# Optimization experiments

Hardware: AMD Instinct MI355X
Metric: run time of the kernel (lower is better)

The kernel has to match this reference:

```python
import jax, jax.numpy as jnp
import numpy as np

E = 23   # unique_experts_num
K = 3    # act_experts_num
D = 1024 # in_features
H = 768  # hidden_features (0.75 * dim, per MOEBlock mlp_ratio)


def setup_inputs() -> dict:
    key = jax.random.key(0)
    ks = jax.random.split(key, 12)
    s_in = 1.0 / np.sqrt(D)
    s_hid = 1.0 / np.sqrt(H)
    x = jax.random.normal(ks[0], (4, 1024, D), dtype=jnp.float32)
    gate_W = jax.random.normal(ks[1], (D, E), dtype=jnp.float32) * s_in
    gate_b = jnp.zeros((E,), jnp.float32)
    bias = jnp.zeros((E,), jnp.float32)  # registered buffer, init to zeros
    W1 = jax.random.normal(ks[2], (E, D, H), dtype=jnp.float32) * s_in
    b1 = jnp.zeros((E, H), jnp.float32)
    W2 = jax.random.normal(ks[3], (E, H, D), dtype=jnp.float32) * s_hid
    b2 = jnp.zeros((E, D), jnp.float32)
    sW1 = jax.random.normal(ks[4], (D, H), dtype=jnp.float32) * s_in
    sb1 = jnp.zeros((H,), jnp.float32)
    sW2 = jax.random.normal(ks[5], (H, D), dtype=jnp.float32) * s_hid
    sb2 = jnp.zeros((D,), jnp.float32)
    return {"x": x, "gate_W": gate_W, "gate_b": gate_b, "bias": bias,
            "W1": W1, "b1": b1, "W2": W2, "b2": b2,
            "sW1": sW1, "sb1": sb1, "sW2": sW2, "sb2": sb2}


def reference(x, gate_W, gate_b, bias, W1, b1, W2, b2, sW1, sb1, sW2, sb2):
    o_shape = x.shape
    xt = x.reshape(-1, o_shape[-1])          # [T, D]
    T = xt.shape[0]

    # gating: sigmoid gate, top-k indices chosen on (gate + bias), weights gathered from gate
    gate = jax.nn.sigmoid(xt @ gate_W + gate_b)            # [T, E]
    _, top_idx = jax.lax.top_k(gate + bias, K)             # [T, K]
    top_w = jnp.take_along_axis(gate, top_idx, axis=-1)    # [T, K]
    top_w = top_w / jnp.sum(top_w, axis=-1, keepdims=True)

    # combine matrix: C[t, e] = normalized gate weight if e in top-k of token t else 0
    C = jnp.zeros((T, E), xt.dtype).at[jnp.arange(T)[:, None], top_idx].set(top_w)

    # all-expert dense compute (math-equivalent to dispatch/compute/combine)
    h = jax.nn.gelu(jnp.einsum('td,edh->eth', xt, W1) + b1[:, None, :], approximate=False)
    y = jnp.einsum('eth,ehd->etd', h, W2) + b2[:, None, :]  # [E, T, D]
    moe_out = jnp.einsum('etd,te->td', y, C)                # weighted combine

    # shared expert applied to every token
    shared = jax.nn.gelu(xt @ sW1 + sb1, approximate=False) @ sW2 + sb2
    out = shared + moe_out

    # aux load-balance loss
    gate_norm = gate / jnp.sum(gate, axis=-1, keepdims=True)
    P = jnp.mean(gate_norm, axis=0)                          # [E]
    counts = jnp.sum(jax.nn.one_hot(top_idx, E, dtype=jnp.float32), axis=(0, 1))  # [E]
    F = E * counts / (K * T)
    aux_loss = jnp.sum(P * F)

    return out.reshape(o_shape), aux_loss, counts.astype(jnp.int32)
```

## Files before the change

### kernel.cpp

```cpp
#include <hip/hip_runtime.h>
#include <math.h>

#define TT 4096
#define DD 1024
#define HH 768
#define NE 23
#define NG 24
#define BM 128
#define BN 128
#define BK 64
#define MAXT 160
#define KB1 16
#define KB2 12
#define NY1 6
#define NY2 8
#define NWG1 (MAXT*NY1)
#define NWG2 (MAXT*NY2)

#define WS_CURS   0
#define WS_COUNTS 512
#define WS_PSUM   544
#define WS_OFFS   576
#define WS_TOFFS  608
#define WS_TOTAL  640
#define WS_T2E    672
#define WS_T2A    832
#define WS_TOKE   1024
#define WS_TOKW   13312
#define WS_LTOK   25600
#define WS_LW     41984
#define WS_PPART  58368
#define WS_CPART  81920
#define WS_SIDX   106496
#define XB_OFF  ((size_t)524288)
#define H_OFF   ((size_t)8912896)
#define W1B_OFF ((size_t)34078720)
#define W2B_OFF ((size_t)71827456)

typedef short bf16x8 __attribute__((ext_vector_type(8)));
typedef float f32x4 __attribute__((ext_vector_type(4)));
typedef unsigned short u16x8 __attribute__((ext_vector_type(8)));

#define S_BARRIER() asm volatile("s_barrier" ::: "memory")
#define WAIT_VM0()  asm volatile("s_waitcnt vmcnt(0)" ::: "memory")

__device__ inline unsigned short bfr(float f) {
    unsigned u = __float_as_uint(f);
    u += 0x7fffu + ((u >> 16) & 1u);
    return (unsigned short)(u >> 16);
}
__device__ inline float b2f(unsigned short u) {
    return __uint_as_float((unsigned)u << 16);
}

__device__ __forceinline__ void gl_lds16(const void* g, void* l) {
    __builtin_amdgcn_global_load_lds(
        (const __attribute__((address_space(1))) unsigned int*)g,
        (__attribute__((address_space(3))) unsigned int*)l, 16, 0, 0);
}

__global__ __launch_bounds__(256) void k_gate(
    const float* __restrict__ x, const float* __restrict__ gW,
    const float* __restrict__ gb, const float* __restrict__ bias,
    int* __restrict__ tokE, float* __restrict__ tokW,
    float* __restrict__ Ppart, int* __restrict__ Cpart,
    unsigned short* __restrict__ xb)
{
    __shared__ float xs[4][DD];
    __shared__ float gv[4][NE];
    __shared__ float ginvs[4];
    __shared__ int sel[4][3];
    const int tid = threadIdx.x;
    const int t0 = blockIdx.x * 4;
    {
        const float4* src = (const float4*)(x + (size_t)t0 * DD);
        float4* dst = (float4*)&xs[0][0];
        #pragma unroll
        for (int i = 0; i < 4; i++) dst[tid + 256 * i] = src[tid + 256 * i];
    }
    __syncthreads();
    {
        const float* xf = &xs[0][0];
        unsigned short* xd = xb + (size_t)t0 * DD;
        #pragma unroll
        for (int it = 0; it < 4; it++) {
            int o = it * 1024 + tid * 4;
            ushort4 u = make_ushort4(bfr(xf[o]), bfr(xf[o + 1]), bfr(xf[o + 2]), bfr(xf[o + 3]));
            *(ushort4*)(xd + o) = u;
        }
    }
    const int w = tid >> 6, l = tid & 63;
    const int t = t0 + w;
    if (l < NE) {
        float s0 = 0.f, s1 = 0.f, s2 = 0.f, s3 = 0.f;
        const float* xw = xs[w];
        for (int d = 0; d < DD; d += 4) {
            s0 = fmaf(xw[d + 0], gW[(d + 0) * NE + l], s0);
            s1 = fmaf(xw[d + 1], gW[(d + 1) * NE + l], s1);
            s2 = fmaf(xw[d + 2], gW[(d + 2) * NE + l], s2);
            s3 = fmaf(xw[d + 3], gW[(d + 3) * NE + l], s3);
        }
        float s = (s0 + s1) + (s2 + s3) + gb[l];
        gv[w][l] = 1.f / (1.f + expf(-s));
    }
    __syncthreads();
    if (l == 0) {
        unsigned chosen = 0;
        int be[3]; float bw[3];
        float gsum = 0.f;
        for (int e = 0; e < NE; e++) gsum += gv[w][e];
        #pragma unroll
        for (int k = 0; k < 3; k++) {
            float m = -1e30f; int mi = 0;
            for (int e = 0; e < NE; e++) {
                float kv = gv[w][e] + bias[e];
                if (!((chosen >> e) & 1u) && kv > m) { m = kv; mi = e; }
            }
            chosen |= 1u << mi;
            be[k] = mi; bw[k] = gv[w][mi];
        }
        float inv = 1.f / (bw[0] + bw[1] + bw[2]);
        #pragma unroll
        for (int k = 0; k < 3; k++) {
            tokE[t * 3 + k] = be[k];
            tokW[t * 3 + k] = bw[k] * inv;
            sel[w][k] = be[k];
        }
        ginvs[w] = 1.f / gsum;
    }
    __syncthreads();
    if (tid < NE) {
        float p = gv[0][tid] * ginvs[0] + gv[1][tid] * ginvs[1]
                + gv[2][tid] * ginvs[2] + gv[3][tid] * ginvs[3];
        Ppart[tid * 1024 + blockIdx.x] = p;
        int c = 0;
        #pragma unroll
        for (int w2 = 0; w2 < 4; w2++)
            #pragma unroll
            for (int k = 0; k < 3; k++) c += (sel[w2][k] == tid);
        Cpart[tid * 1024 + blockIdx.x] = c;
    }
}

__global__ __launch_bounds__(256) void k_reduce(
    const float* __restrict__ Ppart, const int* __restrict__ Cpart,
    int* __restrict__ counts, float* __restrict__ Psum)
{
    const int e = blockIdx.x;
    const int tid = threadIdx.x;
    float s = 0.f; int c = 0;
    for (int i = tid; i < 1024; i += 256) {
        s += Ppart[e * 1024 + i];
        c += Cpart[e * 1024 + i];
    }
    #pragma unroll
    for (int off = 32; off >= 1; off >>= 1) {
        s += __shfl_down(s, off, 64);
        c += __shfl_down(c, off, 64);
    }
    __shared__ float ss[4]; __shared__ int sc[4];
    if ((tid & 63) == 0) { ss[tid >> 6] = s; sc[tid >> 6] = c; }
    __syncthreads();
    if (tid == 0) {
        Psum[e] = ss[0] + ss[1] + ss[2] + ss[3];
        counts[e] = sc[0] + sc[1] + sc[2] + sc[3];
    }
}

__global__ void k_scan(const int* __restrict__ counts, const float* __restrict__ Psum,
                       int* __restrict__ offs, int* __restrict__ toffs,
                       int* __restrict__ total, int* __restrict__ t2e,
                       int* __restrict__ t2a, float* __restrict__ outAux)
{
    if (threadIdx.x != 0 || blockIdx.x != 0) return;
    int off = 0, toff = 0;
    for (int e = 0; e < NG; e++) {
        int c = (e < NE) ? counts[e] : TT;
        offs[e] = off; toffs[e] = toff;
        int nt = (c + BM - 1) / BM;
        for (int t = 0; t < nt; t++) {
            t2e[toff + t] = e;
            t2a[toff + t] = off + t * BM;
        }
        off += c; toff += nt;
    }
    offs[NG] = off; toffs[NG] = toff;
    *total = toff;
    float aux = 0.f;
    for (int e = 0; e < NE; e++) {
        float P = Psum[e] / (float)TT;
        float F = (float)NE * (float)counts[e] / (float)(3 * TT);
        aux += P * F;
    }
    outAux[0] = aux;
    for (int e = 0; e < NE; e++) outAux[1 + e] = (float)counts[e];
}

__global__ void k_scatter(const int* __restrict__ tokE, const float* __restrict__ tokW,
                          const int* __restrict__ offs, int* __restrict__ curs,
                          int* __restrict__ ltok, float* __restrict__ lw,
                          int* __restrict__ sidx)
{
    int t = blockIdx.x * 256 + threadIdx.x;
    if (t >= TT) return;
    #pragma unroll
    for (int k = 0; k < 3; k++) {
        int e = tokE[t * 3 + k];
        int pos = atomicAdd(&curs[e * 16], 1);
        int idx = offs[e] + pos;
        ltok[idx] = t; lw[idx] = tokW[t * 3 + k];
        sidx[t * 3 + k] = idx;
    }
    ltok[3 * TT + t] = t;
    lw[3 * TT + t] = 1.f;
}

__global__ __launch_bounds__(256) void k_cvt_w(
    const float* __restrict__ W, const float* __restrict__ Ws,
    int K, int N, unsigned short* __restrict__ dst)
{
    const int e = blockIdx.z, kb = blockIdx.y;
    const int KBt = gridDim.y;
    const int n0 = blockIdx.x * 64;
    const float* src = (e < NE) ? (W + (size_t)e * K * N) : Ws;
    __shared__ unsigned short Ls[64][66];
    const int tid = threadIdx.x;
    const int c = (tid & 15) * 4, r0 = tid >> 4;
    #pragma unroll
    for (int pass = 0; pass < 4; pass++) {
        int row = pass * 16 + r0;
        float4 v = *(const float4*)(src + (size_t)(kb * 64 + row) * N + n0 + c);
        ushort4 u = make_ushort4(bfr(v.x), bfr(v.y), bfr(v.z), bfr(v.w));
        *(ushort4*)&Ls[row][c] = u;
    }
    __syncthreads();
    unsigned short* dbase = dst + ((size_t)(e * KBt + kb) * N + n0) * 64;
    #pragma unroll
    for (int half = 0; half < 2; half++) {
        int g = half * 256 + tid;
        int n = g >> 3, p = g & 7;
        int j = p ^ (n & 7);
        u16x8 u;
        #pragma unroll
        for (int i = 0; i < 8; i++) u[i] = Ls[j * 8 + i][n];
        *(u16x8*)(dbase + n * 64 + p * 8) = u;
    }
}

__global__ __launch_bounds__(256) void k_mm1(
    const unsigned short* __restrict__ xb, const unsigned short* __restrict__ W1b,
    const float* __restrict__ b1, const float* __restrict__ sb1,
    const int* __restrict__ t2e, const int* __restrict__ t2a,
    const int* __restrict__ offs, const int* __restrict__ total,
    const int* __restrict__ ltok, unsigned short* __restrict__ H)
{
    const int id = blockIdx.x;
    const int wg = (id & 7) * (NWG1 / 8) + (id >> 3);
    const int ns = wg / MAXT;
    const int tb = wg % MAXT;
    if (tb >= *total) return;
    const int e = t2e[tb];
    const int a0 = t2a[tb];
    const int acount = min(offs[e + 1] - a0, BM);
    const float* bb = (e < NE) ? (b1 + e * HH) : sb1;
    const int nb = ns * BN;

    __shared__ unsigned short As[2][BM * BK];
    __shared__ unsigned short Bs[2][BN * BK];
    __shared__ int rows[BM];
    const int tid = threadIdx.x;
    if (tid < BM) rows[tid] = ltok[a0 + min(tid, acount - 1)];
    __syncthreads();

    const int wid = tid >> 6, lane = tid & 63;
    const int wr = wid >> 1, wc = wid & 1;
    const int l15 = lane & 15, l4 = lane >> 4;

    float bv[4];
    #pragma unroll
    for (int n = 0; n < 4; n++) bv[n] = bb[nb + wc * 64 + n * 16 + l15];

    f32x4 acc[4][4];
    #pragma unroll
    for (int m = 0; m < 4; m++)
        #pragma unroll
        for (int n = 0; n < 4; n++) acc[m][n] = (f32x4){0.f, 0.f, 0.f, 0.f};

    const unsigned short* aSrc[4];
    int Goff[4];
    #pragma unroll
    for (int c = 0; c < 4; c++) {
        int G = (wid * 4 + c) * 64 + lane;
        int row = G >> 3, j = G & 7;
        aSrc[c] = xb + (size_t)rows[row] * DD + ((j ^ (row & 7)) << 3);
        Goff[c] = G * 8;
    }
    const unsigned short* wbase = W1b + ((size_t)e * KB1 * HH + nb) * 64;

    auto stage = [&](int buf, int kb) {
        #pragma unroll
        for (int c = 0; c < 4; c++)
            gl_lds16(aSrc[c] + kb * 64, &As[buf][Goff[c]]);
        const unsigned short* wb = wbase + (size_t)kb * (HH * 64);
        #pragma unroll
        for (int c = 0; c < 4; c++)
            gl_lds16(wb + Goff[c], &Bs[buf][Goff[c]]);
    };
    auto compute = [&](int buf) {
        #pragma unroll
        for (int kh = 0; kh < 2; kh++) {
            bf16x8 af[4], bf[4];
            #pragma unroll
            for (int f = 0; f < 4; f++) {
                int ar = wr * 64 + f * 16 + l15;
                int br = wc * 64 + f * 16 + l15;
                int pg = (kh << 2) + l4;
                af[f] = *(const bf16x8*)&As[buf][ar * 64 + ((pg ^ (ar & 7)) << 3)];
                bf[f] = *(const bf16x8*)&Bs[buf][br * 64 + ((pg ^ (br & 7)) << 3)];
            }
            #pragma unroll
            for (int m = 0; m < 4; m++)
                #pragma unroll
                for (int n = 0; n < 4; n++)
                    acc[m][n] = __builtin_amdgcn_mfma_f32_16x16x32_bf16(af[m], bf[n], acc[m][n], 0, 0, 0);
        }
    };

    stage(0, 0);
    WAIT_VM0();
    S_BARRIER();
    int cur = 0;
    #pragma unroll 1
    for (int kb = 0; kb < KB1; kb++) {
        if (kb + 1 < KB1) stage(cur ^ 1, kb + 1);
        __builtin_amdgcn_sched_barrier(0);
        compute(cur);
        if (kb + 1 < KB1) {
            WAIT_VM0();
            S_BARRIER();
            cur ^= 1;
        }
    }

    #pragma unroll
    for (int m = 0; m < 4; m++) {
        int rbase = wr * 64 + m * 16 + l4 * 4;
        #pragma unroll
        for (int n = 0; n < 4; n++) {
            int col = nb + wc * 64 + n * 16 + l15;
            #pragma unroll
            for (int i = 0; i < 4; i++) {
                int r = rbase + i;
                if (r < acount) {
                    float v = acc[m][n][i] + bv[n];
                    float u = v + 0.044715f * v * v * v;
                    float g = v / (1.f + __expf(-1.5957691216f * u));
                    H[(size_t)(a0 + r) * HH + col] = bfr(g);
                }
            }
        }
    }
}

__global__ __launch_bounds__(256) void k_mm2(
    const unsigned short* __restrict__ H, const unsigned short* __restrict__ W2b,
    const float* __restrict__ b2, const float* __restrict__ sb2,
    const int* __restrict__ t2e, const int* __restrict__ t2a,
    const int* __restrict__ offs, const int* __restrict__ total,
    const int* __restrict__ ltok, const float* __restrict__ lw,
    unsigned short* __restrict__ yslot, float* __restrict__ out)
{
    const int id = blockIdx.x;
    const int wg = (id & 7) * (NWG2 / 8) + (id >> 3);
    const int ns = wg / MAXT;
    const int tb = wg % MAXT;
    if (tb >= *total) return;
    const int e = t2e[tb];
    const int a0 = t2a[tb];
    const int acount = min(offs[e + 1] - a0, BM);
    const float* bb = (e < NE) ? (b2 + e * DD) : sb2;
    const int nb = ns * BN;

    __shared__ unsigned short As[2][BM * BK];
    __shared__ unsigned short Bs[2][BN * BK];
    __shared__ int rows[BM];
    __shared__ float wts[BM];
    const int tid = threadIdx.x;
    if (tid < BM) {
        rows[tid] = (tid < acount) ? ltok[a0 + tid] : -1;
        wts[tid]  = (tid < acount) ? lw[a0 + tid] : 0.f;
    }
    __syncthreads();

    const int wid = tid >> 6, lane = tid & 63;
    const int wr = wid >> 1, wc = wid & 1;
    const int l15 = lane & 15, l4 = lane >> 4;

    float bv[4];
    #pragma unroll
    for (int n = 0; n < 4; n++) bv[n] = bb[nb + wc * 64 + n * 16 + l15];

    f32x4 acc[4][4];
    #pragma unroll
    for (int m = 0; m < 4; m++)
        #pragma unroll
        for (int n = 0; n < 4; n++) acc[m][n] = (f32x4){0.f, 0.f, 0.f, 0.f};

    const unsigned short* aSrc[4];
    int Goff[4];
    #pragma unroll
    for (int c = 0; c < 4; c++) {
        int G = (wid * 4 + c) * 64 + lane;
        int row = G >> 3, j = G & 7;
        aSrc[c] = H + (size_t)(a0 + row) * HH + ((j ^ (row & 7)) << 3);
        Goff[c] = G * 8;
    }
    const unsigned short* wbase = W2b + ((size_t)e * KB2 * DD + nb) * 64;

    auto stage = [&](int buf, int kb) {
        #pragma unroll
        for (int c = 0; c < 4; c++)
            gl_lds16(aSrc[c] + kb * 64, &As[buf][Goff[c]]);
        const unsigned short* wb = wbase + (size_t)kb * (DD * 64);
        #pragma unroll
        for (int c = 0; c < 4; c++)
            gl_lds16(wb + Goff[c], &Bs[buf][Goff[c]]);
    };
    auto compute = [&](int buf) {
        #pragma unroll
        for (int kh = 0; kh < 2; kh++) {
            bf16x8 af[4], bf[4];
            #pragma unroll
            for (int f = 0; f < 4; f++) {
                int ar = wr * 64 + f * 16 + l15;
                int br = wc * 64 + f * 16 + l15;
                int pg = (kh << 2) + l4;
                af[f] = *(const bf16x8*)&As[buf][ar * 64 + ((pg ^ (ar & 7)) << 3)];
                bf[f] = *(const bf16x8*)&Bs[buf][br * 64 + ((pg ^ (br & 7)) << 3)];
            }
            #pragma unroll
            for (int m = 0; m < 4; m++)
                #pragma unroll
                for (int n = 0; n < 4; n++)
                    acc[m][n] = __builtin_amdgcn_mfma_f32_16x16x32_bf16(af[m], bf[n], acc[m][n], 0, 0, 0);
        }
    };

    stage(0, 0);
    WAIT_VM0();
    S_BARRIER();
    int cur = 0;
    #pragma unroll 1
    for (int kb = 0; kb < KB2; kb++) {
        if (kb + 1 < KB2) stage(cur ^ 1, kb + 1);
        __builtin_amdgcn_sched_barrier(0);
        compute(cur);
        if (kb + 1 < KB2) {
            WAIT_VM0();
            S_BARRIER();
            cur ^= 1;
        }
    }

    if (e == NE) {
        #pragma unroll
        for (int m = 0; m < 4; m++) {
            int rbase = wr * 64 + m * 16 + l4 * 4;
            #pragma unroll
            for (int n = 0; n < 4; n++) {
                int col = nb + wc * 64 + n * 16 + l15;
                #pragma unroll
                for (int i = 0; i < 4; i++) {
                    int r = rbase + i;
                    out[(size_t)rows[r] * DD + col] = acc[m][n][i] + bv[n];
                }
            }
        }
    } else {
        #pragma unroll
        for (int m = 0; m < 4; m++) {
            int rbase = wr * 64 + m * 16 + l4 * 4;
            #pragma unroll
            for (int n = 0; n < 4; n++) {
                int col = nb + wc * 64 + n * 16 + l15;
                #pragma unroll
                for (int i = 0; i < 4; i++) {
                    int r = rbase + i;
                    if (r < acount)
                        yslot[(size_t)(a0 + r) * DD + col] = bfr(wts[r] * (acc[m][n][i] + bv[n]));
                }
            }
        }
    }
}

__global__ __launch_bounds__(256) void k_combine(
    const unsigned short* __restrict__ yslot, const int* __restrict__ sidx,
    float* __restrict__ out)
{
    const int t = blockIdx.x;
    const int s0 = sidx[t * 3 + 0], s1 = sidx[t * 3 + 1], s2 = sidx[t * 3 + 2];
    const int d = threadIdx.x * 4;
    float* o = out + (size_t)t * DD + d;
    float4 v = *(float4*)o;
    ushort4 a = *(const ushort4*)(yslot + (size_t)s0 * DD + d);
    ushort4 b = *(const ushort4*)(yslot + (size_t)s1 * DD + d);
    ushort4 c = *(const ushort4*)(yslot + (size_t)s2 * DD + d);
    v.x += b2f(a.x) + b2f(b.x) + b2f(c.x);
    v.y += b2f(a.y) + b2f(b.y) + b2f(c.y);
    v.z += b2f(a.z) + b2f(b.z) + b2f(c.z);
    v.w += b2f(a.w) + b2f(b.w) + b2f(c.w);
    *(float4*)o = v;
}

extern "C" void kernel_launch(void* const* d_in, const int* in_sizes, int n_in,
                              void* d_out, int out_size, void* d_ws, size_t ws_size,
                              hipStream_t stream)
{
    const float* x    = (const float*)d_in[0];
    const float* gW   = (const float*)d_in[1];
    const float* gb   = (const float*)d_in[2];
    const float* bias = (const float*)d_in[3];
    const float* W1   = (const float*)d_in[4];
    const float* b1   = (const float*)d_in[5];
    const float* W2   = (const float*)d_in[6];
    const float* b2   = (const float*)d_in[7];
    const float* sW1  = (const float*)d_in[8];
    const float* sb1  = (const float*)d_in[9];
    const float* sW2  = (const float*)d_in[10];
    const float* sb2  = (const float*)d_in[11];
    float* out = (float*)d_out;
    float* wsf = (float*)d_ws;
    int*   wsi = (int*)d_ws;

    hipMemsetAsync(d_ws, 0, 2048, stream);

    int*   curs   = wsi + WS_CURS;
    int*   counts = wsi + WS_COUNTS;
    float* Psum   = wsf + WS_PSUM;
    int*   offs   = wsi + WS_OFFS;
    int*   toffs  = wsi + WS_TOFFS;
    int*   total  = wsi + WS_TOTAL;
    int*   t2e    = wsi + WS_T2E;
    int*   t2a    = wsi + WS_T2A;
    int*   tokE   = wsi + WS_TOKE;
    float* tokW   = wsf + WS_TOKW;
    int*   ltok   = wsi + WS_LTOK;
    float* lwt    = wsf + WS_LW;
    float* Ppart  = wsf + WS_PPART;
    int*   Cpart  = wsi + WS_CPART;
    int*   sidx   = wsi + WS_SIDX;
    unsigned short* xb  = (unsigned short*)((char*)d_ws + XB_OFF);
    unsigned short* Hb  = (unsigned short*)((char*)d_ws + H_OFF);
    unsigned short* W1b = (unsigned short*)((char*)d_ws + W1B_OFF);
    unsigned short* W2b = (unsigned short*)((char*)d_ws + W2B_OFF);
    unsigned short* yslot = W1b;

    k_cvt_w<<<dim3(HH / 64, DD / 64, NG), 256, 0, stream>>>(W1, sW1, DD, HH, W1b);
    k_cvt_w<<<dim3(DD / 64, HH / 64, NG), 256, 0, stream>>>(W2, sW2, HH, DD, W2b);
    k_gate<<<TT / 4, 256, 0, stream>>>(x, gW, gb, bias, tokE, tokW, Ppart, Cpart, xb);
    k_reduce<<<NE, 256, 0, stream>>>(Ppart, Cpart, counts, Psum);
    k_scan<<<1, 64, 0, stream>>>(counts, Psum, offs, toffs, total, t2e, t2a,
                                 out + (size_t)TT * DD);
    k_scatter<<<TT / 256, 256, 0, stream>>>(tokE, tokW, offs, curs, ltok, lwt, sidx);
    k_mm1<<<NWG1, 256, 0, stream>>>(xb, W1b, b1, sb1, t2e, t2a, offs, total, ltok, Hb);
    k_mm2<<<NWG2, 256, 0, stream>>>(Hb, W2b, b2, sb2, t2e, t2a, offs, total, ltok, lwt,
                                    yslot, out);
    k_combine<<<TT, 256, 0, stream>>>(yslot, sidx, out);
}
```

Measured before the change: 230.9 us.

## Use 256-row tiles with 512 threads and triple-buffered LDS in expert GEMMs

Both grouped expert GEMMs move from 128x128 to 256x128 tiles with 8 waves per workgroup, which halves the weight-tile reloads per token row. The software pipeline goes from double to triple buffering: two stages are prefetched and the loop waits with vmcnt(6) so one k-block load can stay in flight during compute. In exchange, per-expert padding grows because the last tile of each expert is larger, there are fewer workgroups, and LDS use rises to about 147KB, which limits occupancy to one workgroup per CU.

```diff
diff --git a/kernel.cpp b/kernel.cpp
--- a/kernel.cpp
+++ b/kernel.cpp
@@ -6,10 +6,10 @@
 #define HH 768
 #define NE 23
 #define NG 24
-#define BM 128
+#define BM 256
 #define BN 128
 #define BK 64
-#define MAXT 160
+#define MAXT 88
 #define KB1 16
 #define KB2 12
 #define NY1 6
@@ -42,6 +42,7 @@
 typedef unsigned short u16x8 __attribute__((ext_vector_type(8)));
 
 #define S_BARRIER() asm volatile("s_barrier" ::: "memory")
+#define WAIT_VM6()  asm volatile("s_waitcnt vmcnt(6)" ::: "memory")
 #define WAIT_VM0()  asm volatile("s_waitcnt vmcnt(0)" ::: "memory")
 
 __device__ inline unsigned short bfr(float f) {
@@ -247,7 +248,7 @@
     }
 }
 
-__global__ __launch_bounds__(256) void k_mm1(
+__global__ __launch_bounds__(512) void k_mm1(
     const unsigned short* __restrict__ xb, const unsigned short* __restrict__ W1b,
     const float* __restrict__ b1, const float* __restrict__ sb1,
     const int* __restrict__ t2e, const int* __restrict__ t2a,
@@ -265,15 +266,15 @@
     const float* bb = (e < NE) ? (b1 + e * HH) : sb1;
     const int nb = ns * BN;
 
-    __shared__ unsigned short As[2][BM * BK];
-    __shared__ unsigned short Bs[2][BN * BK];
+    __shared__ unsigned short As[3][BM * BK];
+    __shared__ unsigned short Bs[3][BN * BK];
     __shared__ int rows[BM];
     const int tid = threadIdx.x;
     if (tid < BM) rows[tid] = ltok[a0 + min(tid, acount - 1)];
     __syncthreads();
 
     const int wid = tid >> 6, lane = tid & 63;
-    const int wr = wid >> 1, wc = wid & 1;
+    const int wr = wid & 3, wc = wid >> 2;
     const int l15 = lane & 15, l4 = lane >> 4;
 
     float bv[4];
@@ -287,24 +288,26 @@
         for (int n = 0; n < 4; n++) acc[m][n] = (f32x4){0.f, 0.f, 0.f, 0.f};
 
     const unsigned short* aSrc[4];
-    int Goff[4];
+    int GA[4], GB[2];
     #pragma unroll
     for (int c = 0; c < 4; c++) {
-        int G = (wid * 4 + c) * 64 + lane;
+        int G = c * 512 + tid;
         int row = G >> 3, j = G & 7;
         aSrc[c] = xb + (size_t)rows[row] * DD + ((j ^ (row & 7)) << 3);
-        Goff[c] = G * 8;
-    }
+        GA[c] = G * 8;
+    }
+    #pragma unroll
+    for (int c = 0; c < 2; c++) GB[c] = (c * 512 + tid) * 8;
     const unsigned short* wbase = W1b + ((size_t)e * KB1 * HH + nb) * 64;
 
     auto stage = [&](int buf, int kb) {
         #pragma unroll
         for (int c = 0; c < 4; c++)
-            gl_lds16(aSrc[c] + kb * 64, &As[buf][Goff[c]]);
+            gl_lds16(aSrc[c] + kb * 64, &As[buf][GA[c]]);
         const unsigned short* wb = wbase + (size_t)kb * (HH * 64);
         #pragma unroll
-        for (int c = 0; c < 4; c++)
-            gl_lds16(wb + Goff[c], &Bs[buf][Goff[c]]);
+        for (int c = 0; c < 2; c++)
+            gl_lds16(wb + GB[c], &Bs[buf][GB[c]]);
     };
     auto compute = [&](int buf) {
         #pragma unroll
@@ -327,19 +330,21 @@
     };
 
     stage(0, 0);
-    WAIT_VM0();
+    stage(1, 1);
+    WAIT_VM6();
     S_BARRIER();
     int cur = 0;
     #pragma unroll 1
     for (int kb = 0; kb < KB1; kb++) {
-        if (kb + 1 < KB1) stage(cur ^ 1, kb + 1);
+        if (kb + 2 < KB1) stage((cur + 2) % 3, kb + 2);
         __builtin_amdgcn_sched_barrier(0);
         compute(cur);
         if (kb + 1 < KB1) {
-            WAIT_VM0();
+            if (kb + 2 < KB1) WAIT_VM6();
+            else              WAIT_VM0();
             S_BARRIER();
-            cur ^= 1;
-        }
+        }
+        cur = (cur == 2) ? 0 : cur + 1;
     }
 
     #pragma unroll
@@ -362,7 +367,7 @@
     }
 }
 
-__global__ __launch_bounds__(256) void k_mm2(
+__global__ __launch_bounds__(512) void k_mm2(
     const unsigned short* __restrict__ H, const unsigned short* __restrict__ W2b,
     const float* __restrict__ b2, const float* __restrict__ sb2,
     const int* __restrict__ t2e, const int* __restrict__ t2a,
@@ -381,8 +386,8 @@
     const float* bb = (e < NE) ? (b2 + e * DD) : sb2;
     const int nb = ns * BN;
 
-    __shared__ unsigned short As[2][BM * BK];
-    __shared__ unsigned short Bs[2][BN * BK];
+    __shared__ unsigned short As[3][BM * BK];
+    __shared__ unsigned short Bs[3][BN * BK];
     __shared__ int rows[BM];
     __shared__ float wts[BM];
     const int tid = threadIdx.x;
@@ -393,7 +398,7 @@
     __syncthreads();
 
     const int wid = tid >> 6, lane = tid & 63;
-    const int wr = wid >> 1, wc = wid & 1;
+    const int wr = wid & 3, wc = wid >> 2;
     const int l15 = lane & 15, l4 = lane >> 4;
 
     float bv[4];
@@ -407,24 +412,26 @@
         for (int n = 0; n < 4; n++) acc[m][n] = (f32x4){0.f, 0.f, 0.f, 0.f};
 
     const unsigned short* aSrc[4];
-    int Goff[4];
+    int GA[4], GB[2];
     #pragma unroll
     for (int c = 0; c < 4; c++) {
-        int G = (wid * 4 + c) * 64 + lane;
+        int G = c * 512 + tid;
         int row = G >> 3, j = G & 7;
         aSrc[c] = H + (size_t)(a0 + row) * HH + ((j ^ (row & 7)) << 3);
-        Goff[c] = G * 8;
-    }
+        GA[c] = G * 8;
+    }
+    #pragma unroll
+    for (int c = 0; c < 2; c++) GB[c] = (c * 512 + tid) * 8;
     const unsigned short* wbase = W2b + ((size_t)e * KB2 * DD + nb) * 64;
 
     auto stage = [&](int buf, int kb) {
         #pragma unroll
         for (int c = 0; c < 4; c++)
-            gl_lds16(aSrc[c] + kb * 64, &As[buf][Goff[c]]);
+            gl_lds16(aSrc[c] + kb * 64, &As[buf][GA[c]]);
         const unsigned short* wb = wbase + (size_t)kb * (DD * 64);
         #pragma unroll
-        for (int c = 0; c < 4; c++)
-            gl_lds16(wb + Goff[c], &Bs[buf][Goff[c]]);
+        for (int c = 0; c < 2; c++)
+            gl_lds16(wb + GB[c], &Bs[buf][GB[c]]);
     };
     auto compute = [&](int buf) {
         #pragma unroll
@@ -447,19 +454,21 @@
     };
 
     stage(0, 0);
-    WAIT_VM0();
+    stage(1, 1);
+    WAIT_VM6();
     S_BARRIER();
     int cur = 0;
     #pragma unroll 1
     for (int kb = 0; kb < KB2; kb++) {
-        if (kb + 1 < KB2) stage(cur ^ 1, kb + 1);
+        if (kb + 2 < KB2) stage((cur + 2) % 3, kb + 2);
         __builtin_amdgcn_sched_barrier(0);
         compute(cur);
         if (kb + 1 < KB2) {
-            WAIT_VM0();
+            if (kb + 2 < KB2) WAIT_VM6();
+            else              WAIT_VM0();
             S_BARRIER();
-            cur ^= 1;
-        }
+        }
+        cur = (cur == 2) ? 0 : cur + 1;
     }
 
     if (e == NE) {
@@ -563,8 +572,8 @@
     k_scan<<<1, 64, 0, stream>>>(counts, Psum, offs, toffs, total, t2e, t2a,
                                  out + (size_t)TT * DD);
     k_scatter<<<TT / 256, 256, 0, stream>>>(tokE, tokW, offs, curs, ltok, lwt, sidx);
-    k_mm1<<<NWG1, 256, 0, stream>>>(xb, W1b, b1, sb1, t2e, t2a, offs, total, ltok, Hb);
-    k_mm2<<<NWG2, 256, 0, stream>>>(Hb, W2b, b2, sb2, t2e, t2a, offs, total, ltok, lwt,
+    k_mm1<<<NWG1, 512, 0, stream>>>(xb, W1b, b1, sb1, t2e, t2a, offs, total, ltok, Hb);
+    k_mm2<<<NWG2, 512, 0, stream>>>(Hb, W2b, b2, sb2, t2e, t2a, offs, total, ltok, lwt,
                                     yslot, out);
     k_combine<<<TT, 256, 0, stream>>>(yslot, sidx, out);
 }
```

Measured after the change: 267.0 us. 15.6% more time.

## Fuse weight conversion and gating into one launch, drop memset

Applied to the files above, without the earlier changes.

Merges the two bf16 weight-conversion kernels and the gating kernel into one launch. Each conversion block now handles two 64-row k-tiles and packs pairs of rows into 32-bit words for wider LDS and global stores. The workspace memset is removed: the scatter cursors are now zeroed inside the scan kernel, and counts and Psum move to new offsets. This saves launch overhead and lets gating overlap with the weight conversion, at the cost of a larger LDS footprint shared between the two block roles.

```diff
diff --git a/kernel.cpp b/kernel.cpp
--- a/kernel.cpp
+++ b/kernel.cpp
@@ -16,12 +16,12 @@
 #define NY2 8
 #define NWG1 (MAXT*NY1)
 #define NWG2 (MAXT*NY2)
+#define CVT1_BLKS 2304
+#define CVT_TOT   4608
+#define GATE_BLKS 1024
 
 #define WS_CURS   0
-#define WS_COUNTS 512
-#define WS_PSUM   544
 #define WS_OFFS   576
-#define WS_TOFFS  608
 #define WS_TOTAL  640
 #define WS_T2E    672
 #define WS_T2A    832
@@ -39,7 +39,6 @@
 
 typedef short bf16x8 __attribute__((ext_vector_type(8)));
 typedef float f32x4 __attribute__((ext_vector_type(4)));
-typedef unsigned short u16x8 __attribute__((ext_vector_type(8)));
 
 #define S_BARRIER() asm volatile("s_barrier" ::: "memory")
 #define WAIT_VM0()  asm volatile("s_waitcnt vmcnt(0)" ::: "memory")
@@ -49,6 +48,9 @@
     u += 0x7fffu + ((u >> 16) & 1u);
     return (unsigned short)(u >> 16);
 }
+__device__ inline unsigned bfr2(float lo, float hi) {
+    return (unsigned)bfr(lo) | ((unsigned)bfr(hi) << 16);
+}
 __device__ inline float b2f(unsigned short u) {
     return __uint_as_float((unsigned)u << 16);
 }
@@ -59,24 +61,80 @@
         (__attribute__((address_space(3))) unsigned int*)l, 16, 0, 0);
 }
 
-__global__ __launch_bounds__(256) void k_gate(
+__global__ __launch_bounds__(256) void k_gatecvt(
     const float* __restrict__ x, const float* __restrict__ gW,
     const float* __restrict__ gb, const float* __restrict__ bias,
+    const float* __restrict__ W1, const float* __restrict__ sW1,
+    const float* __restrict__ W2, const float* __restrict__ sW2,
     int* __restrict__ tokE, float* __restrict__ tokW,
     float* __restrict__ Ppart, int* __restrict__ Cpart,
-    unsigned short* __restrict__ xb)
-{
-    __shared__ float xs[4][DD];
-    __shared__ float gv[4][NE];
-    __shared__ float ginvs[4];
-    __shared__ int sel[4][3];
+    unsigned short* __restrict__ xb,
+    unsigned short* __restrict__ W1b, unsigned short* __restrict__ W2b)
+{
+    __shared__ __align__(16) char smem[16896];
     const int tid = threadIdx.x;
-    const int t0 = blockIdx.x * 4;
+
+    if (blockIdx.x < CVT_TOT) {
+        int id = blockIdx.x;
+        const float* src; unsigned short* dst;
+        int N, kb0, n0, KBt, e;
+        if (id < CVT1_BLKS) {
+            N = HH; KBt = KB1;
+            n0 = (id % 12) * 64; kb0 = ((id / 12) % 8) * 2; e = id / 96;
+            src = (e < NE) ? (W1 + (size_t)e * DD * HH) : sW1;
+            dst = W1b;
+        } else {
+            id -= CVT1_BLKS;
+            N = DD; KBt = KB2;
+            n0 = (id % 16) * 64; kb0 = ((id / 16) % 6) * 2; e = id / 96;
+            src = (e < NE) ? (W2 + (size_t)e * HH * DD) : sW2;
+            dst = W2b;
+        }
+        unsigned (*Ls)[32][65] = (unsigned (*)[32][65])smem;
+        const int c = (tid & 15) * 4, r2l = tid >> 4;
+        #pragma unroll
+        for (int t = 0; t < 2; t++) {
+            const float* tsrc = src + (size_t)(kb0 + t) * 64 * N + n0;
+            #pragma unroll
+            for (int pass = 0; pass < 2; pass++) {
+                int row2 = pass * 16 + r2l;
+                float4 v0 = *(const float4*)(tsrc + (size_t)(2 * row2) * N + c);
+                float4 v1 = *(const float4*)(tsrc + (size_t)(2 * row2 + 1) * N + c);
+                uint4 o;
+                o.x = bfr2(v0.x, v1.x); o.y = bfr2(v0.y, v1.y);
+                o.z = bfr2(v0.z, v1.z); o.w = bfr2(v0.w, v1.w);
+                *(uint4*)&Ls[t][row2][c] = o;
+            }
+        }
+        __syncthreads();
+        #pragma unroll
+        for (int t = 0; t < 2; t++) {
+            unsigned short* dbase = dst + ((size_t)(e * KBt + kb0 + t) * N + n0) * 64;
+            #pragma unroll
+            for (int half = 0; half < 2; half++) {
+                int g = half * 256 + tid;
+                int n = g >> 3, p = g & 7;
+                int j4 = (p ^ (n & 7)) * 4;
+                uint4 o;
+                o.x = Ls[t][j4 + 0][n]; o.y = Ls[t][j4 + 1][n];
+                o.z = Ls[t][j4 + 2][n]; o.w = Ls[t][j4 + 3][n];
+                *(uint4*)(dbase + n * 64 + p * 8) = o;
+            }
+        }
+        return;
+    }
+
+    float (*xs)[DD] = (float (*)[DD])smem;
+    float (*gv)[NE] = (float (*)[NE])(smem + 16384);
+    float* ginvs    = (float*)(smem + 16768);
+    int (*sel)[3]   = (int (*)[3])(smem + 16784);
+    const int bid = blockIdx.x - CVT_TOT;
+    const int t0 = bid * 4;
     {
-        const float4* src = (const float4*)(x + (size_t)t0 * DD);
-        float4* dst = (float4*)&xs[0][0];
-        #pragma unroll
-        for (int i = 0; i < 4; i++) dst[tid + 256 * i] = src[tid + 256 * i];
+        const float4* srcx = (const float4*)(x + (size_t)t0 * DD);
+        float4* dstx = (float4*)&xs[0][0];
+        #pragma unroll
+        for (int i = 0; i < 4; i++) dstx[tid + 256 * i] = srcx[tid + 256 * i];
     }
     __syncthreads();
     {
@@ -132,13 +190,13 @@
     if (tid < NE) {
         float p = gv[0][tid] * ginvs[0] + gv[1][tid] * ginvs[1]
                 + gv[2][tid] * ginvs[2] + gv[3][tid] * ginvs[3];
-        Ppart[tid * 1024 + blockIdx.x] = p;
+        Ppart[tid * 1024 + bid] = p;
         int c = 0;
         #pragma unroll
         for (int w2 = 0; w2 < 4; w2++)
             #pragma unroll
             for (int k = 0; k < 3; k++) c += (sel[w2][k] == tid);
-        Cpart[tid * 1024 + blockIdx.x] = c;
+        Cpart[tid * 1024 + bid] = c;
     }
 }
 
@@ -168,15 +226,17 @@
 }
 
 __global__ void k_scan(const int* __restrict__ counts, const float* __restrict__ Psum,
-                       int* __restrict__ offs, int* __restrict__ toffs,
-                       int* __restrict__ total, int* __restrict__ t2e,
-                       int* __restrict__ t2a, float* __restrict__ outAux)
-{
-    if (threadIdx.x != 0 || blockIdx.x != 0) return;
+                       int* __restrict__ offs, int* __restrict__ total,
+                       int* __restrict__ t2e, int* __restrict__ t2a,
+                       int* __restrict__ curs, float* __restrict__ outAux)
+{
+    const int tid = threadIdx.x;
+    for (int i = tid; i < NE * 16; i += 256) curs[i] = 0;
+    if (tid != 0) return;
     int off = 0, toff = 0;
     for (int e = 0; e < NG; e++) {
         int c = (e < NE) ? counts[e] : TT;
-        offs[e] = off; toffs[e] = toff;
+        offs[e] = off;
         int nt = (c + BM - 1) / BM;
         for (int t = 0; t < nt; t++) {
             t2e[toff + t] = e;
@@ -184,7 +244,7 @@
         }
         off += c; toff += nt;
     }
-    offs[NG] = off; toffs[NG] = toff;
+    offs[NG] = off;
     *total = toff;
     float aux = 0.f;
     for (int e = 0; e < NE; e++) {
@@ -213,38 +273,6 @@
     }
     ltok[3 * TT + t] = t;
     lw[3 * TT + t] = 1.f;
-}
-
-__global__ __launch_bounds__(256) void k_cvt_w(
-    const float* __restrict__ W, const float* __restrict__ Ws,
-    int K, int N, unsigned short* __restrict__ dst)
-{
-    const int e = blockIdx.z, kb = blockIdx.y;
-    const int KBt = gridDim.y;
-    const int n0 = blockIdx.x * 64;
-    const float* src = (e < NE) ? (W + (size_t)e * K * N) : Ws;
-    __shared__ unsigned short Ls[64][66];
-    const int tid = threadIdx.x;
-    const int c = (tid & 15) * 4, r0 = tid >> 4;
-    #pragma unroll
-    for (int pass = 0; pass < 4; pass++) {
-        int row = pass * 16 + r0;
-        float4 v = *(const float4*)(src + (size_t)(kb * 64 + row) * N + n0 + c);
-        ushort4 u = make_ushort4(bfr(v.x), bfr(v.y), bfr(v.z), bfr(v.w));
-        *(ushort4*)&Ls[row][c] = u;
-    }
-    __syncthreads();
-    unsigned short* dbase = dst + ((size_t)(e * KBt + kb) * N + n0) * 64;
-    #pragma unroll
-    for (int half = 0; half < 2; half++) {
-        int g = half * 256 + tid;
-        int n = g >> 3, p = g & 7;
-        int j = p ^ (n & 7);
-        u16x8 u;
-        #pragma unroll
-        for (int i = 0; i < 8; i++) u[i] = Ls[j * 8 + i][n];
-        *(u16x8*)(dbase + n * 64 + p * 8) = u;
-    }
 }
 
 __global__ __launch_bounds__(256) void k_mm1(
@@ -533,13 +561,8 @@
     float* wsf = (float*)d_ws;
     int*   wsi = (int*)d_ws;
 
-    hipMemsetAsync(d_ws, 0, 2048, stream);
-
     int*   curs   = wsi + WS_CURS;
-    int*   counts = wsi + WS_COUNTS;
-    float* Psum   = wsf + WS_PSUM;
     int*   offs   = wsi + WS_OFFS;
-    int*   toffs  = wsi + WS_TOFFS;
     int*   total  = wsi + WS_TOTAL;
     int*   t2e    = wsi + WS_T2E;
     int*   t2a    = wsi + WS_T2A;
@@ -550,18 +573,19 @@
     float* Ppart  = wsf + WS_PPART;
     int*   Cpart  = wsi + WS_CPART;
     int*   sidx   = wsi + WS_SIDX;
+    int*   counts = wsi + 432;
+    float* Psum   = wsf + 464;
     unsigned short* xb  = (unsigned short*)((char*)d_ws + XB_OFF);
     unsigned short* Hb  = (unsigned short*)((char*)d_ws + H_OFF);
     unsigned short* W1b = (unsigned short*)((char*)d_ws + W1B_OFF);
     unsigned short* W2b = (unsigned short*)((char*)d_ws + W2B_OFF);
     unsigned short* yslot = W1b;
 
-    k_cvt_w<<<dim3(HH / 64, DD / 64, NG), 256, 0, stream>>>(W1, sW1, DD, HH, W1b);
-    k_cvt_w<<<dim3(DD / 64, HH / 64, NG), 256, 0, stream>>>(W2, sW2, HH, DD, W2b);
-    k_gate<<<TT / 4, 256, 0, stream>>>(x, gW, gb, bias, tokE, tokW, Ppart, Cpart, xb);
+    k_gatecvt<<<CVT_TOT + GATE_BLKS, 256, 0, stream>>>(
+        x, gW, gb, bias, W1, sW1, W2, sW2, tokE, tokW, Ppart, Cpart, xb, W1b, W2b);
     k_reduce<<<NE, 256, 0, stream>>>(Ppart, Cpart, counts, Psum);
-    k_scan<<<1, 64, 0, stream>>>(counts, Psum, offs, toffs, total, t2e, t2a,
-                                 out + (size_t)TT * DD);
+    k_scan<<<1, 256, 0, stream>>>(counts, Psum, offs, total, t2e, t2a, curs,
+                                  out + (size_t)TT * DD);
     k_scatter<<<TT / 256, 256, 0, stream>>>(tokE, tokW, offs, curs, ltok, lwt, sidx);
     k_mm1<<<NWG1, 256, 0, stream>>>(xb, W1b, b1, sb1, t2e, t2a, offs, total, ltok, Hb);
     k_mm2<<<NWG2, 256, 0, stream>>>(Hb, W2b, b2, sb2, t2e, t2a, offs, total, ltok, lwt,
```

Result: faster. 225.5 us (-2.4%).
